# Kernel optimization log

Measured on AMD Instinct MI355X. Metric: run time of the kernel, lower is better.

Reference implementation:

```python
import jax, jax.numpy as jnp
import numpy as np

B, T_Q, T_KV, D = 4, 2048, 4096, 1024
H = 16
HD = D // H  # head_dim = 64
EPS_LN = 1e-5
EPS_NORM = 1e-12


def setup_inputs() -> dict:
    key = jax.random.key(0)
    ks = jax.random.split(key, 12)
    inp = {
        'query': jax.random.normal(ks[0], (B, T_Q, D), jnp.float32),
        'key':   jax.random.normal(ks[1], (B, T_KV, D), jnp.float32),
        'value': jax.random.normal(ks[2], (B, T_KV, D), jnp.float32),
        # projections (nn.Linear stores weight as [out, in]; y = x @ W.T)
        'Wq': jax.random.normal(ks[3], (D, D), jnp.float32) * 0.02,
        'Wk': jax.random.normal(ks[4], (D, D), jnp.float32) * 0.02,
        'Wv': jax.random.normal(ks[5], (D, D), jnp.float32) * 0.02,
        'Wo': jax.random.normal(ks[6], (D, D), jnp.float32) * 0.01,
        'bo': jnp.zeros((D,), jnp.float32),
        'Wbeta':  jax.random.normal(ks[7], (H, D), jnp.float32) * 0.02,
        'bbeta':  jnp.zeros((H,), jnp.float32),
        'Walpha': jax.random.normal(ks[8], (H, D), jnp.float32) * 0.02,
        'balpha': jnp.full((H,), -1.0, jnp.float32),
        # per-head-dim LayerNorms
        'gq': jnp.ones((HD,), jnp.float32),
        'bq': jnp.zeros((HD,), jnp.float32),
        'gk': jnp.ones((HD,), jnp.float32),
        'bk': jnp.zeros((HD,), jnp.float32),
    }
    return inp


def _layernorm(x, g, b):
    mu = jnp.mean(x, axis=-1, keepdims=True)
    var = jnp.mean(jnp.square(x - mu), axis=-1, keepdims=True)
    return (x - mu) * jax.lax.rsqrt(var + EPS_LN) * g + b


def reference(query, key, value, Wq, Wk, Wv, Wo, bo,
              Wbeta, bbeta, Walpha, balpha, gq, bq, gk, bk):
    Bq, Tq, Dm = query.shape
    Tkv = key.shape[1]

    q = (query @ Wq.T).reshape(Bq, Tq, H, HD)
    k = (key   @ Wk.T).reshape(Bq, Tkv, H, HD)
    v = (value @ Wv.T).reshape(Bq, Tkv, H, HD)

    q = _layernorm(q, gq, bq)
    k = _layernorm(k, gk, bk)
    # F.normalize(k, dim=-1)
    k = k / jnp.maximum(jnp.linalg.norm(k, axis=-1, keepdims=True), EPS_NORM)

    beta  = jax.nn.sigmoid(key @ Wbeta.T  + bbeta)   # [B, Tkv, H]
    alpha = jax.nn.sigmoid(key @ Walpha.T + balpha)  # [B, Tkv, H]

    # time-major for scan: [Tkv, B, H, ...]
    k_t = jnp.moveaxis(k, 1, 0)
    v_t = jnp.moveaxis(v, 1, 0)
    b_t = jnp.moveaxis(beta, 1, 0)
    a_t = jnp.moveaxis(alpha, 1, 0)

    M0 = jnp.zeros((Bq, H, HD, HD), query.dtype)

    def step(M, inputs):
        kt, vt, bt, at = inputs  # [B,H,d],[B,H,d],[B,H],[B,H]
        Mk = jnp.einsum('bhij,bhj->bhi', M, kt)
        erase = at[..., None, None] * jnp.einsum('bhi,bhj->bhij', Mk, kt)
        write = bt[..., None, None] * jnp.einsum('bhi,bhj->bhij', vt, kt)
        return M - erase + write, None

    M, _ = jax.lax.scan(step, M0, (k_t, v_t, b_t, a_t))

    # out[b,t,h,i] = sum_j M[b,h,i,j] * q[b,t,h,j]
    out = jnp.einsum('bhij,bthj->bthi', M, q).reshape(Bq, Tq, Dm)
    out = out @ Wo.T + bo  # dropout is identity in eval mode
    return out
```

## Files before the change

kernel.cpp:

```cpp
#include <hip/hip_runtime.h>
#include <math.h>

#define TQ_LEN 2048
#define TKV_LEN 4096
#define BATCH 4
#define DMODEL 1024
#define NH 16
#define HD 64
#define NKBA 1152
#define CCH 128
#define NCHUNK (TKV_LEN / CCH)

typedef unsigned short u16;
typedef __attribute__((ext_vector_type(8))) short bf16x8;
typedef __attribute__((ext_vector_type(4))) float f32x4;

__device__ __forceinline__ u16 f2bf(float x) {
  union { float f; unsigned u; } c; c.f = x;
  unsigned r = c.u + 0x7fffu + ((c.u >> 16) & 1u);
  return (u16)(r >> 16);
}
__device__ __forceinline__ float bf2f(u16 x) {
  union { unsigned u; float f; } c; c.u = ((unsigned)x) << 16;
  return c.f;
}

__device__ __forceinline__ float wave_sum64(float x) {
#pragma unroll
  for (int off = 32; off; off >>= 1) x += __shfl_xor(x, off, 64);
  return x;
}

__global__ __launch_bounds__(256) void cvt_bf16_kernel(
    const float* __restrict__ s, u16* __restrict__ d) {
  size_t i = ((size_t)blockIdx.x * 256 + threadIdx.x) * 8;
  float4 a = *(const float4*)&s[i];
  float4 b = *(const float4*)&s[i + 4];
  union { u16 h[8]; uint4 v; } o;
  o.h[0] = f2bf(a.x); o.h[1] = f2bf(a.y); o.h[2] = f2bf(a.z); o.h[3] = f2bf(a.w);
  o.h[4] = f2bf(b.x); o.h[5] = f2bf(b.y); o.h[6] = f2bf(b.z); o.h[7] = f2bf(b.w);
  *(uint4*)&d[i] = o.v;
}

__global__ __launch_bounds__(256) void wcat_bf_kernel(
    const float* __restrict__ Wk, const float* __restrict__ Wb,
    const float* __restrict__ Wa, u16* __restrict__ Wcat) {
  int i = blockIdx.x * 256 + threadIdx.x;
  int row = i / DMODEL, col = i % DMODEL;
  float v;
  if (row < 1024)      v = Wk[i];
  else if (row < 1040) v = Wb[(row - 1024) * DMODEL + col];
  else if (row < 1056) v = Wa[(row - 1040) * DMODEL + col];
  else                 v = 0.f;
  Wcat[i] = f2bf(v);
}

__device__ __forceinline__ void stage_tile_bf16(
    const u16* __restrict__ G, int ldg, int row0, int kcol0,
    u16* lds, int wid, int lane) {
#pragma unroll
  for (int e = 0; e < 2; ++e) {
    int r = (wid * 2 + e) * 16;
    const u16* g = G + (size_t)(row0 + r + (lane >> 2)) * ldg + kcol0 + (lane & 3) * 8;
    __builtin_amdgcn_global_load_lds(
        (const __attribute__((address_space(1))) void*)g,
        (__attribute__((address_space(3))) void*)(lds + r * 32), 16, 0, 0);
  }
}

template <bool HAS_BIAS, bool OUT_BF16>
__global__ __launch_bounds__(256) void gemm_bt_bf16(
    const u16* __restrict__ A, const u16* __restrict__ B,
    const float* __restrict__ bias, void* __restrict__ Cv,
    int M, int N, int K, int ldc) {
  __shared__ u16 Al[2][128 * 32];
  __shared__ u16 Bl[2][128 * 32];
  const int tid = threadIdx.x;
  const int wid = tid >> 6, lane = tid & 63;
  const int wr = wid >> 1, wc = wid & 1;
  const int bm = blockIdx.y * 128, bn = blockIdx.x * 128;
  const int lrow = lane & 15, lk = (lane >> 4) * 8;

  int aoff[4], boff[4];
#pragma unroll
  for (int f = 0; f < 4; ++f) {
    aoff[f] = (wr * 64 + f * 16 + lrow) * 32 + lk;
    boff[f] = (wc * 64 + f * 16 + lrow) * 32 + lk;
  }

  f32x4 acc[4][4] = {};
  const int nk = K >> 5;
  int cur = 0;
  stage_tile_bf16(A, K, bm, 0, &Al[0][0], wid, lane);
  stage_tile_bf16(B, K, bn, 0, &Bl[0][0], wid, lane);
  __syncthreads();
  for (int kt = 0; kt < nk; ++kt) {
    if (kt + 1 < nk) {
      stage_tile_bf16(A, K, bm, (kt + 1) * 32, &Al[cur ^ 1][0], wid, lane);
      stage_tile_bf16(B, K, bn, (kt + 1) * 32, &Bl[cur ^ 1][0], wid, lane);
    }
    bf16x8 af[4], bfr[4];
#pragma unroll
    for (int f = 0; f < 4; ++f) af[f] = *(const bf16x8*)&Al[cur][aoff[f]];
#pragma unroll
    for (int f = 0; f < 4; ++f) bfr[f] = *(const bf16x8*)&Bl[cur][boff[f]];
#pragma unroll
    for (int mf = 0; mf < 4; ++mf)
#pragma unroll
      for (int nf = 0; nf < 4; ++nf)
        acc[mf][nf] = __builtin_amdgcn_mfma_f32_16x16x32_bf16(
            af[mf], bfr[nf], acc[mf][nf], 0, 0, 0);
    __syncthreads();
    cur ^= 1;
  }
  const int crow0 = bm + wr * 64 + (lane >> 4) * 4;
  const int ccol0 = bn + wc * 64 + (lane & 15);
#pragma unroll
  for (int mf = 0; mf < 4; ++mf)
#pragma unroll
    for (int nf = 0; nf < 4; ++nf) {
      int col = ccol0 + nf * 16;
      float bv = HAS_BIAS ? bias[col] : 0.f;
#pragma unroll
      for (int i = 0; i < 4; ++i) {
        int row = crow0 + mf * 16 + i;
        float vout = acc[mf][nf][i] + bv;
        if (OUT_BF16)
          ((u16*)Cv)[(size_t)row * ldc + col] = f2bf(vout);
        else
          ((float*)Cv)[(size_t)row * ldc + col] = vout;
      }
    }
}

__global__ __launch_bounds__(256) void ln_q_kernel(float* __restrict__ q,
                                                   const float* __restrict__ g,
                                                   const float* __restrict__ b) {
  int gidx = blockIdx.x * 4 + (threadIdx.x >> 6);
  int lane = threadIdx.x & 63;
  int row = gidx >> 4, h = gidx & 15;
  float* p = q + (size_t)row * DMODEL + h * HD + lane;
  float x = *p;
  float mu = wave_sum64(x) * (1.f / 64.f);
  float d = x - mu;
  float var = wave_sum64(d * d) * (1.f / 64.f);
  float y = d * rsqrtf(var + 1e-5f) * g[lane] + b[lane];
  *p = y;
}

__global__ __launch_bounds__(256) void ln_k_kernel(float* __restrict__ kb,
                                                   const float* __restrict__ g,
                                                   const float* __restrict__ b) {
  int gidx = blockIdx.x * 4 + (threadIdx.x >> 6);
  int lane = threadIdx.x & 63;
  int row = gidx >> 4, h = gidx & 15;
  float* p = kb + (size_t)row * NKBA + h * HD + lane;
  float x = *p;
  float mu = wave_sum64(x) * (1.f / 64.f);
  float d = x - mu;
  float var = wave_sum64(d * d) * (1.f / 64.f);
  float y = d * rsqrtf(var + 1e-5f) * g[lane] + b[lane];
  float s2 = wave_sum64(y * y);
  y = y / fmaxf(sqrtf(s2), 1e-12f);
  *p = y;
}

__global__ __launch_bounds__(256) void sig_kernel(
    const float* __restrict__ kb, const float* __restrict__ bb,
    const float* __restrict__ ba, float* __restrict__ beta,
    float* __restrict__ alpha) {
  int i = blockIdx.x * 256 + threadIdx.x;
  int row = i >> 4, h = i & 15;
  float lb = kb[(size_t)row * NKBA + 1024 + h] + bb[h];
  float la = kb[(size_t)row * NKBA + 1040 + h] + ba[h];
  beta[i]  = 1.f / (1.f + expf(-lb));
  alpha[i] = 1.f / (1.f + expf(-la));
}

__global__ __launch_bounds__(64, 2) void chunk_scan_kernel(
    const float* __restrict__ kb, const u16* __restrict__ v,
    const float* __restrict__ beta, const float* __restrict__ alpha,
    float* __restrict__ Pbuf, float* __restrict__ Sbuf) {
  __shared__ float klds[2][64];
  int slot = blockIdx.x;
  int bh = slot / NCHUNK, ck = slot % NCHUNK;
  int b = bh >> 4, h = bh & 15;
  int lane = threadIdx.x;
  int t0 = ck * CCH;
  const float* kbase = kb + ((size_t)b * TKV_LEN + t0) * NKBA + h * HD;
  const u16* vbase = v + ((size_t)b * TKV_LEN + t0) * DMODEL + h * HD;
  const float* bbase = beta + ((size_t)b * TKV_LEN + t0) * NH + h;
  const float* abase = alpha + ((size_t)b * TKV_LEN + t0) * NH + h;

  float P[64], S[64];
#pragma unroll
  for (int j = 0; j < 64; ++j) { P[j] = (j == lane) ? 1.f : 0.f; S[j] = 0.f; }

  klds[0][lane] = kbase[lane];
  float kn = kbase[(size_t)NKBA + lane];
  float vn = bf2f(vbase[lane]);
  float btn = bbase[0];
  float atn = abase[0];

  for (int t = 0; t < CCH; ++t) {
    float vc = vn, bt = btn, at = atn;
    if (t + 1 < CCH) {
      vn = bf2f(vbase[(size_t)(t + 1) * DMODEL + lane]);
      btn = bbase[(size_t)(t + 1) * NH];
      atn = abase[(size_t)(t + 1) * NH];
    }
    float kn2 = (t + 2 < CCH) ? kbase[(size_t)(t + 2) * NKBA + lane] : 0.f;
    __syncthreads();
    klds[(t + 1) & 1][lane] = kn;
    float4 kk[16];
#pragma unroll
    for (int j4 = 0; j4 < 16; ++j4) kk[j4] = *(const float4*)&klds[t & 1][j4 * 4];
    float pka[4] = {0.f, 0.f, 0.f, 0.f}, ska[4] = {0.f, 0.f, 0.f, 0.f};
#pragma unroll
    for (int j4 = 0; j4 < 16; ++j4) {
      pka[0] = fmaf(P[4 * j4 + 0], kk[j4].x, pka[0]);
      pka[1] = fmaf(P[4 * j4 + 1], kk[j4].y, pka[1]);
      pka[2] = fmaf(P[4 * j4 + 2], kk[j4].z, pka[2]);
      pka[3] = fmaf(P[4 * j4 + 3], kk[j4].w, pka[3]);
      ska[0] = fmaf(S[4 * j4 + 0], kk[j4].x, ska[0]);
      ska[1] = fmaf(S[4 * j4 + 1], kk[j4].y, ska[1]);
      ska[2] = fmaf(S[4 * j4 + 2], kk[j4].z, ska[2]);
      ska[3] = fmaf(S[4 * j4 + 3], kk[j4].w, ska[3]);
    }
    float pk = (pka[0] + pka[1]) + (pka[2] + pka[3]);
    float sk = (ska[0] + ska[1]) + (ska[2] + ska[3]);
    float cp = -at * pk;
    float cs = bt * vc - at * sk;
#pragma unroll
    for (int j4 = 0; j4 < 16; ++j4) {
      P[4 * j4 + 0] = fmaf(cp, kk[j4].x, P[4 * j4 + 0]);
      P[4 * j4 + 1] = fmaf(cp, kk[j4].y, P[4 * j4 + 1]);
      P[4 * j4 + 2] = fmaf(cp, kk[j4].z, P[4 * j4 + 2]);
      P[4 * j4 + 3] = fmaf(cp, kk[j4].w, P[4 * j4 + 3]);
      S[4 * j4 + 0] = fmaf(cs, kk[j4].x, S[4 * j4 + 0]);
      S[4 * j4 + 1] = fmaf(cs, kk[j4].y, S[4 * j4 + 1]);
      S[4 * j4 + 2] = fmaf(cs, kk[j4].z, S[4 * j4 + 2]);
      S[4 * j4 + 3] = fmaf(cs, kk[j4].w, S[4 * j4 + 3]);
    }
    kn = kn2;
  }
  float* po = Pbuf + (size_t)slot * 4096 + (size_t)lane * 64;
  float* so = Sbuf + (size_t)slot * 4096 + (size_t)lane * 64;
#pragma unroll
  for (int j4 = 0; j4 < 16; ++j4) {
    *(float4*)&po[j4 * 4] = make_float4(P[4 * j4], P[4 * j4 + 1], P[4 * j4 + 2], P[4 * j4 + 3]);
    *(float4*)&so[j4 * 4] = make_float4(S[4 * j4], S[4 * j4 + 1], S[4 * j4 + 2], S[4 * j4 + 3]);
  }
}

__global__ __launch_bounds__(256) void fold_kernel(
    const float* __restrict__ Pin, const float* __restrict__ Sin,
    float* __restrict__ Pout, float* __restrict__ Sout, int nitems) {
  __shared__ float Pa[64][68], Sa[64][68], Pc[64][68], Sc[64][68];
  const int tid = threadIdx.x;
  const int r0 = (tid >> 4) * 4, c0 = (tid & 15) * 4;
  for (int l = tid; l < 4096; l += 256) {
    int r = l >> 6, c = l & 63;
    Pa[r][c] = (r == c) ? 1.f : 0.f;
    Sa[r][c] = 0.f;
  }
  for (int item = 0; item < nitems; ++item) {
    const float* pg = Pin + ((size_t)blockIdx.x * nitems + item) * 4096;
    const float* sg = Sin + ((size_t)blockIdx.x * nitems + item) * 4096;
#pragma unroll
    for (int e = 0; e < 4; ++e) {
      int l = tid * 16 + e * 4;
      int r = l >> 6, c = l & 63;
      *(float4*)&Pc[r][c] = *(const float4*)&pg[l];
      *(float4*)&Sc[r][c] = *(const float4*)&sg[l];
    }
    __syncthreads();
    float accP[4][4] = {}, accS[4][4] = {};
#pragma unroll 4
    for (int j4 = 0; j4 < 16; ++j4) {
      float bmat[4][4];
#pragma unroll
      for (int jj = 0; jj < 4; ++jj) {
        float4 t = *(const float4*)&Pc[j4 * 4 + jj][c0];
        bmat[jj][0] = t.x; bmat[jj][1] = t.y; bmat[jj][2] = t.z; bmat[jj][3] = t.w;
      }
#pragma unroll
      for (int rr = 0; rr < 4; ++rr) {
        float4 tp = *(const float4*)&Pa[r0 + rr][j4 * 4];
        float4 ts = *(const float4*)&Sa[r0 + rr][j4 * 4];
        float ap[4] = {tp.x, tp.y, tp.z, tp.w};
        float as[4] = {ts.x, ts.y, ts.z, ts.w};
#pragma unroll
        for (int jj = 0; jj < 4; ++jj)
#pragma unroll
          for (int cc = 0; cc < 4; ++cc) {
            accP[rr][cc] = fmaf(ap[jj], bmat[jj][cc], accP[rr][cc]);
            accS[rr][cc] = fmaf(as[jj], bmat[jj][cc], accS[rr][cc]);
          }
      }
    }
#pragma unroll
    for (int rr = 0; rr < 4; ++rr)
#pragma unroll
      for (int cc = 0; cc < 4; ++cc) accS[rr][cc] += Sc[r0 + rr][c0 + cc];
    __syncthreads();
#pragma unroll
    for (int rr = 0; rr < 4; ++rr)
#pragma unroll
      for (int cc = 0; cc < 4; ++cc) {
        Pa[r0 + rr][c0 + cc] = accP[rr][cc];
        Sa[r0 + rr][c0 + cc] = accS[rr][cc];
      }
  }
  __syncthreads();
  float* po = Pout + (size_t)blockIdx.x * 4096;
  float* so = Sout + (size_t)blockIdx.x * 4096;
#pragma unroll
  for (int e = 0; e < 4; ++e) {
    int l = tid * 16 + e * 4;
    int r = l >> 6, c = l & 63;
    *(float4*)&po[l] = *(const float4*)&Pa[r][c];
    *(float4*)&so[l] = *(const float4*)&Sa[r][c];
  }
}

__global__ __launch_bounds__(256) void outm_kernel(
    const float* __restrict__ Mg, const float* __restrict__ q,
    u16* __restrict__ attn) {
  __shared__ float Ml[64][65];
  int bh = blockIdx.x;
  int tchunk = blockIdx.y;
  int b = bh >> 4, h = bh & 15;
  int tid = threadIdx.x;
  const float* mg = Mg + (size_t)bh * 4096;
#pragma unroll
  for (int e = 0; e < 16; ++e) {
    int l = tid + e * 256;
    Ml[l >> 6][l & 63] = mg[l];
  }
  __syncthreads();
  int lane = tid & 63, tt = tid >> 6;
  const float* qb = q + ((size_t)b * TQ_LEN + tchunk * 256) * DMODEL + h * HD;
  u16* ob = attn + ((size_t)b * TQ_LEN + tchunk * 256) * DMODEL + h * HD;
  for (int it = 0; it < 64; ++it) {
    int t = it * 4 + tt;
    const float* qr = qb + (size_t)t * DMODEL;
    float acc = 0.f;
#pragma unroll
    for (int j4 = 0; j4 < 16; ++j4) {
      float4 qv = *(const float4*)&qr[j4 * 4];
      acc += Ml[lane][j4 * 4 + 0] * qv.x + Ml[lane][j4 * 4 + 1] * qv.y +
             Ml[lane][j4 * 4 + 2] * qv.z + Ml[lane][j4 * 4 + 3] * qv.w;
    }
    ob[(size_t)t * DMODEL + lane] = f2bf(acc);
  }
}

extern "C" void kernel_launch(void* const* d_in, const int* in_sizes, int n_in,
                              void* d_out, int out_size, void* d_ws,
                              size_t ws_size, hipStream_t stream) {
  const float* query = (const float*)d_in[0];
  const float* key   = (const float*)d_in[1];
  const float* value = (const float*)d_in[2];
  const float* Wq    = (const float*)d_in[3];
  const float* Wk    = (const float*)d_in[4];
  const float* Wv    = (const float*)d_in[5];
  const float* Wo    = (const float*)d_in[6];
  const float* bo    = (const float*)d_in[7];
  const float* Wbeta = (const float*)d_in[8];
  const float* bbeta = (const float*)d_in[9];
  const float* Walpha= (const float*)d_in[10];
  const float* balpha= (const float*)d_in[11];
  const float* gq    = (const float*)d_in[12];
  const float* bq    = (const float*)d_in[13];
  const float* gk    = (const float*)d_in[14];
  const float* bk    = (const float*)d_in[15];
  float* out = (float*)d_out;

  const int MQ = BATCH * TQ_LEN;
  const int MKV = BATCH * TKV_LEN;
  const int NSLOT = 64 * NCHUNK;

  float* ws = (float*)d_ws;
  size_t off = 0;
  u16* Wcat_bf = (u16*)(ws + off); off += (size_t)NKBA * DMODEL / 2;
  u16* Wq_bf   = (u16*)(ws + off); off += (size_t)DMODEL * DMODEL / 2;
  u16* Wv_bf   = (u16*)(ws + off); off += (size_t)DMODEL * DMODEL / 2;
  u16* Wo_bf   = (u16*)(ws + off); off += (size_t)DMODEL * DMODEL / 2;
  u16* qbf = (u16*)(ws + off); size_t qbf_f = off; off += (size_t)MQ * DMODEL / 2;
  u16* kbf = (u16*)(ws + off); size_t kbf_f = off; off += (size_t)MKV * DMODEL / 2;
  u16* vbf = (u16*)(ws + off); size_t vbf_f = off; off += (size_t)MKV * DMODEL / 2;
  float* qp   = ws + off; off += (size_t)MQ * DMODEL;
  float* kba  = ws + off; size_t kba_f = off; off += (size_t)MKV * NKBA;
  u16* vpb = (u16*)(ws + off); off += (size_t)MKV * DMODEL / 2;
  float* Pbuf = ws + kbf_f;
  float* Sbuf = ws + vbf_f;
  float* Gp   = ws + qbf_f;
  float* Gs   = ws + qbf_f + 1048576;
  float* Fp   = ws + qbf_f + 2097152;
  float* beta = ws + qbf_f + 2359296;
  float* alpha= ws + qbf_f + 2621440;
  float* Mg   = ws + qbf_f + 2883584;
  u16* attn_bf = (u16*)(ws + kba_f);

  wcat_bf_kernel<<<NKBA * DMODEL / 256, 256, 0, stream>>>(Wk, Wbeta, Walpha, Wcat_bf);
  cvt_bf16_kernel<<<DMODEL * DMODEL / 2048, 256, 0, stream>>>(Wq, Wq_bf);
  cvt_bf16_kernel<<<DMODEL * DMODEL / 2048, 256, 0, stream>>>(Wv, Wv_bf);
  cvt_bf16_kernel<<<DMODEL * DMODEL / 2048, 256, 0, stream>>>(Wo, Wo_bf);
  cvt_bf16_kernel<<<MQ * DMODEL / 2048, 256, 0, stream>>>(query, qbf);
  cvt_bf16_kernel<<<MKV * DMODEL / 2048, 256, 0, stream>>>(key, kbf);
  cvt_bf16_kernel<<<MKV * DMODEL / 2048, 256, 0, stream>>>(value, vbf);
  gemm_bt_bf16<false, false><<<dim3(DMODEL / 128, MQ / 128), 256, 0, stream>>>(
      qbf, Wq_bf, nullptr, qp, MQ, DMODEL, DMODEL, DMODEL);
  gemm_bt_bf16<false, false><<<dim3(NKBA / 128, MKV / 128), 256, 0, stream>>>(
      kbf, Wcat_bf, nullptr, kba, MKV, NKBA, DMODEL, NKBA);
  gemm_bt_bf16<false, true><<<dim3(DMODEL / 128, MKV / 128), 256, 0, stream>>>(
      vbf, Wv_bf, nullptr, vpb, MKV, DMODEL, DMODEL, DMODEL);
  ln_q_kernel<<<MQ * NH / 4, 256, 0, stream>>>(qp, gq, bq);
  ln_k_kernel<<<MKV * NH / 4, 256, 0, stream>>>(kba, gk, bk);
  sig_kernel<<<MKV * NH / 256, 256, 0, stream>>>(kba, bbeta, balpha, beta, alpha);
  chunk_scan_kernel<<<NSLOT, 64, 0, stream>>>(kba, vpb, beta, alpha, Pbuf, Sbuf);
  fold_kernel<<<NSLOT / 8, 256, 0, stream>>>(Pbuf, Sbuf, Gp, Gs, 8);
  fold_kernel<<<64, 256, 0, stream>>>(Gp, Gs, Fp, Mg, 4);
  outm_kernel<<<dim3(64, TQ_LEN / 256), 256, 0, stream>>>(Mg, qp, attn_bf);
  gemm_bt_bf16<true, false><<<dim3(DMODEL / 128, MQ / 128), 256, 0, stream>>>(
      attn_bf, Wo_bf, bo, out, MQ, DMODEL, DMODEL, DMODEL);
  (void)in_sizes; (void)n_in; (void)out_size; (void)ws_size;
}
```

Measured before the change: 704.6 us.

## Split chunk scan P and S recurrences across two waves per block

```diff
diff --git a/kernel.cpp b/kernel.cpp
--- a/kernel.cpp
+++ b/kernel.cpp
@@ -177,80 +177,75 @@
   alpha[i] = 1.f / (1.f + expf(-la));
 }
 
-__global__ __launch_bounds__(64, 2) void chunk_scan_kernel(
+__global__ __launch_bounds__(128, 4) void chunk_scan_kernel(
     const float* __restrict__ kb, const u16* __restrict__ v,
     const float* __restrict__ beta, const float* __restrict__ alpha,
     float* __restrict__ Pbuf, float* __restrict__ Sbuf) {
-  __shared__ float klds[2][64];
+  __shared__ float klds[4][64];
   int slot = blockIdx.x;
   int bh = slot / NCHUNK, ck = slot % NCHUNK;
   int b = bh >> 4, h = bh & 15;
-  int lane = threadIdx.x;
+  int wid = threadIdx.x >> 6;
+  int lane = threadIdx.x & 63;
   int t0 = ck * CCH;
   const float* kbase = kb + ((size_t)b * TKV_LEN + t0) * NKBA + h * HD;
   const u16* vbase = v + ((size_t)b * TKV_LEN + t0) * DMODEL + h * HD;
   const float* bbase = beta + ((size_t)b * TKV_LEN + t0) * NH + h;
   const float* abase = alpha + ((size_t)b * TKV_LEN + t0) * NH + h;
 
-  float P[64], S[64];
-#pragma unroll
-  for (int j = 0; j < 64; ++j) { P[j] = (j == lane) ? 1.f : 0.f; S[j] = 0.f; }
-
-  klds[0][lane] = kbase[lane];
-  float kn = kbase[(size_t)NKBA + lane];
-  float vn = bf2f(vbase[lane]);
+  float R[64];
+#pragma unroll
+  for (int j = 0; j < 64; ++j) R[j] = (wid == 0 && j == lane) ? 1.f : 0.f;
+
+  float kn = 0.f;
+  if (wid == 0) {
+    klds[0][lane] = kbase[lane];
+    klds[1][lane] = kbase[(size_t)NKBA + lane];
+    kn = (CCH > 2) ? kbase[(size_t)2 * NKBA + lane] : 0.f;
+  }
+  float vn = (wid == 1) ? bf2f(vbase[lane]) : 0.f;
   float btn = bbase[0];
   float atn = abase[0];
 
   for (int t = 0; t < CCH; ++t) {
     float vc = vn, bt = btn, at = atn;
     if (t + 1 < CCH) {
-      vn = bf2f(vbase[(size_t)(t + 1) * DMODEL + lane]);
+      if (wid == 1) vn = bf2f(vbase[(size_t)(t + 1) * DMODEL + lane]);
       btn = bbase[(size_t)(t + 1) * NH];
       atn = abase[(size_t)(t + 1) * NH];
     }
-    float kn2 = (t + 2 < CCH) ? kbase[(size_t)(t + 2) * NKBA + lane] : 0.f;
+    if (wid == 0) {
+      if (t + 2 < CCH) klds[(t + 2) & 3][lane] = kn;
+      kn = (t + 3 < CCH) ? kbase[(size_t)(t + 3) * NKBA + lane] : 0.f;
+    }
     __syncthreads();
-    klds[(t + 1) & 1][lane] = kn;
+    const float* kcur = klds[t & 3];
     float4 kk[16];
 #pragma unroll
-    for (int j4 = 0; j4 < 16; ++j4) kk[j4] = *(const float4*)&klds[t & 1][j4 * 4];
-    float pka[4] = {0.f, 0.f, 0.f, 0.f}, ska[4] = {0.f, 0.f, 0.f, 0.f};
+    for (int j4 = 0; j4 < 16; ++j4) kk[j4] = *(const float4*)&kcur[j4 * 4];
+    float d0 = 0.f, d1 = 0.f, d2 = 0.f, d3 = 0.f;
 #pragma unroll
     for (int j4 = 0; j4 < 16; ++j4) {
-      pka[0] = fmaf(P[4 * j4 + 0], kk[j4].x, pka[0]);
-      pka[1] = fmaf(P[4 * j4 + 1], kk[j4].y, pka[1]);
-      pka[2] = fmaf(P[4 * j4 + 2], kk[j4].z, pka[2]);
-      pka[3] = fmaf(P[4 * j4 + 3], kk[j4].w, pka[3]);
-      ska[0] = fmaf(S[4 * j4 + 0], kk[j4].x, ska[0]);
-      ska[1] = fmaf(S[4 * j4 + 1], kk[j4].y, ska[1]);
-      ska[2] = fmaf(S[4 * j4 + 2], kk[j4].z, ska[2]);
-      ska[3] = fmaf(S[4 * j4 + 3], kk[j4].w, ska[3]);
-    }
-    float pk = (pka[0] + pka[1]) + (pka[2] + pka[3]);
-    float sk = (ska[0] + ska[1]) + (ska[2] + ska[3]);
-    float cp = -at * pk;
-    float cs = bt * vc - at * sk;
+      d0 = fmaf(R[4 * j4 + 0], kk[j4].x, d0);
+      d1 = fmaf(R[4 * j4 + 1], kk[j4].y, d1);
+      d2 = fmaf(R[4 * j4 + 2], kk[j4].z, d2);
+      d3 = fmaf(R[4 * j4 + 3], kk[j4].w, d3);
+    }
+    float dot = (d0 + d1) + (d2 + d3);
+    float c = (wid == 0) ? (-at * dot) : fmaf(bt, vc, -at * dot);
 #pragma unroll
     for (int j4 = 0; j4 < 16; ++j4) {
-      P[4 * j4 + 0] = fmaf(cp, kk[j4].x, P[4 * j4 + 0]);
-      P[4 * j4 + 1] = fmaf(cp, kk[j4].y, P[4 * j4 + 1]);
-      P[4 * j4 + 2] = fmaf(cp, kk[j4].z, P[4 * j4 + 2]);
-      P[4 * j4 + 3] = fmaf(cp, kk[j4].w, P[4 * j4 + 3]);
-      S[4 * j4 + 0] = fmaf(cs, kk[j4].x, S[4 * j4 + 0]);
-      S[4 * j4 + 1] = fmaf(cs, kk[j4].y, S[4 * j4 + 1]);
-      S[4 * j4 + 2] = fmaf(cs, kk[j4].z, S[4 * j4 + 2]);
-      S[4 * j4 + 3] = fmaf(cs, kk[j4].w, S[4 * j4 + 3]);
-    }
-    kn = kn2;
-  }
-  float* po = Pbuf + (size_t)slot * 4096 + (size_t)lane * 64;
-  float* so = Sbuf + (size_t)slot * 4096 + (size_t)lane * 64;
-#pragma unroll
-  for (int j4 = 0; j4 < 16; ++j4) {
-    *(float4*)&po[j4 * 4] = make_float4(P[4 * j4], P[4 * j4 + 1], P[4 * j4 + 2], P[4 * j4 + 3]);
-    *(float4*)&so[j4 * 4] = make_float4(S[4 * j4], S[4 * j4 + 1], S[4 * j4 + 2], S[4 * j4 + 3]);
-  }
+      R[4 * j4 + 0] = fmaf(c, kk[j4].x, R[4 * j4 + 0]);
+      R[4 * j4 + 1] = fmaf(c, kk[j4].y, R[4 * j4 + 1]);
+      R[4 * j4 + 2] = fmaf(c, kk[j4].z, R[4 * j4 + 2]);
+      R[4 * j4 + 3] = fmaf(c, kk[j4].w, R[4 * j4 + 3]);
+    }
+  }
+  float* ro = (wid == 0 ? Pbuf : Sbuf) + (size_t)slot * 4096 + (size_t)lane * 64;
+#pragma unroll
+  for (int j4 = 0; j4 < 16; ++j4)
+    *(float4*)&ro[j4 * 4] =
+        make_float4(R[4 * j4], R[4 * j4 + 1], R[4 * j4 + 2], R[4 * j4 + 3]);
 }
 
 __global__ __launch_bounds__(256) void fold_kernel(
@@ -419,7 +414,7 @@
   ln_q_kernel<<<MQ * NH / 4, 256, 0, stream>>>(qp, gq, bq);
   ln_k_kernel<<<MKV * NH / 4, 256, 0, stream>>>(kba, gk, bk);
   sig_kernel<<<MKV * NH / 256, 256, 0, stream>>>(kba, bbeta, balpha, beta, alpha);
-  chunk_scan_kernel<<<NSLOT, 64, 0, stream>>>(kba, vpb, beta, alpha, Pbuf, Sbuf);
+  chunk_scan_kernel<<<NSLOT, 128, 0, stream>>>(kba, vpb, beta, alpha, Pbuf, Sbuf);
   fold_kernel<<<NSLOT / 8, 256, 0, stream>>>(Pbuf, Sbuf, Gp, Gs, 8);
   fold_kernel<<<64, 256, 0, stream>>>(Gp, Gs, Fp, Mg, 4);
   outm_kernel<<<dim3(64, TQ_LEN / 256), 256, 0, stream>>>(Mg, qp, attn_bf);
```

Measured after the change: 1.360 ms. +93.0%, slower.
